# Performance work log

Measured on AMD Instinct MI355X. Metric: run time of the kernel, lower is better.

Reference implementation:

```python
import jax, jax.numpy as jnp
import numpy as np
import math

EPS = 1e-6
KP = -1.0  # Poincare ball curvature (c=1 -> kappa=-1)
KS = 1.0   # stereographic sphere projection (c=1 -> kappa=+1)

def _n(x):
    return jnp.sqrt(jnp.sum(x * x, -1, keepdims=True) + 1e-15)

def tan_k(u, k):
    if k < 0:
        return jnp.tanh(u)
    return jnp.tan(jnp.clip(u, -1.47079, 1.47079))

def artan_k(u, k):
    if k < 0:
        return jnp.arctanh(jnp.clip(u, -1 + 1e-5, 1 - 1e-5))
    return jnp.arctan(u)

def proj(x, k):
    if k < 0:
        n = _n(x)
        m = 1.0 - 1e-4
        return jnp.where(n > m, x * (m / n), x)
    return x

def expmap0(u, k):
    n = _n(u)
    return proj(tan_k(n, k) * u / n, k)

def logmap0(y, k):
    n = _n(y)
    return artan_k(n, k) * y / n

def _safe_den(d):
    return jnp.where(d >= 0, jnp.maximum(d, EPS), jnp.minimum(d, -EPS))

def mobius_add(x, y, k):
    x2 = jnp.sum(x * x, -1, keepdims=True)
    y2 = jnp.sum(y * y, -1, keepdims=True)
    xy = jnp.sum(x * y, -1, keepdims=True)
    num = (1 - 2 * k * xy - k * y2) * x + (1 + k * x2) * y
    den = 1 - 2 * k * xy + k * k * x2 * y2
    return proj(num / _safe_den(den), k)

def mobius_pw_mul(w, x, k):
    wx = w * x
    nx = _n(x)
    nwx = _n(wx)
    return proj(tan_k(nwx / nx * artan_k(nx, k), k) * wx / nwx, k)

def mobius_smul(r, x, k):
    n = _n(x)
    return proj(tan_k(r * artan_k(n, k), k) * x / n, k)

def wmid(xs, k, axis, w=None):
    lam = 2.0 / (1.0 + k * jnp.sum(xs * xs, -1, keepdims=True))
    if w is None:
        w = jnp.ones_like(lam)
    num = jnp.sum(w * lam * xs, axis=axis)
    den = jnp.abs(jnp.sum(w * (lam - 1.0), axis=axis))
    return mobius_smul(0.5, num / jnp.maximum(den, EPS), k)

def slin(x, W, b, k=None):
    if k is None:
        return x @ W.T + b
    return expmap0(logmap0(x, k) @ W.T + b, k)

def dist(x, y, k):
    return 2.0 * artan_k(_n(mobius_add(-x, y, k))[..., 0], k)

def hyp_attn(kk, q, v, k):
    # kk, v: [N,K,h]; q: [N,h]
    sc = -dist(q[:, None, :], kk, k)              # [N,K]
    a = jax.nn.softmax(sc, axis=1)[..., None]
    return wmid(v, k, axis=1, w=a)

def euc_attn(kk, q, v):
    sc = jnp.einsum('nkh,nh->nk', kk, q) / math.sqrt(kk.shape[-1])
    a = jax.nn.softmax(sc, axis=1)
    return jnp.einsum('nk,nkh->nh', a, v)


def _forward(x, h1, c1, h2, c2, h3, c3, del_t, iou1, iou2, iou3,
             Wq_w, Wq_b, Wc_w, Wc_b, Uf_w, Uf_b, Up_w, Up_b,
             Uiou_w, Uiou_b, d, nbr):
    sg, th = jax.nn.sigmoid, jnp.tanh
    # mailbox gather (message_func + DGL mailbox), [N,K,h]
    mh1, mh2, mh3 = h1[nbr], h2[nbr], h3[nbr]
    mc1, mc2, mc3 = c1[nbr], c2[nbr], c3[nbr]
    g_t = (d / (del_t[nbr] + 1.0))[..., None]      # [N,K,1]

    x_1p = slin(expmap0(x, KP), Wq_w, Wq_b, KP)
    x_1s = slin(expmap0(x, KS), Wq_w, Wq_b, KS)
    x_1e = slin(x, Wq_w, Wq_b)

    s1 = logmap0(sg(slin(mh1, Up_w, Up_b, KP)), KP)
    s2 = logmap0(sg(slin(mh2, Up_w, Up_b, KS)), KS)
    s3 = sg(slin(mh3, Up_w, Up_b))

    ht1p = mobius_pw_mul(s1, mh1, KP)
    ht2p = mobius_pw_mul(s2, expmap0(logmap0(mh2, KS), KP), KP)
    ht3p = mobius_pw_mul(s3, expmap0(mh3, KP), KP)
    h_1p = 3.0 * wmid(jnp.stack([ht1p, ht2p, ht3p]), KP, axis=0)

    ht1s = mobius_pw_mul(s1, expmap0(logmap0(mh1, KP), KS), KP)
    ht2s = mobius_pw_mul(s2, mh2, KS)
    ht3s = mobius_pw_mul(s3, expmap0(mh3, KS), KS)
    h_1s = 3.0 * wmid(jnp.stack([ht1s, ht2s, ht3s]), KP, axis=0)

    ht1e = logmap0(mobius_pw_mul(s1, mh1, KP), KP)
    ht2e = logmap0(mobius_pw_mul(s2, mh2, KS), KS)
    h_1e = ht1e + ht2e + s3 * mh3

    h_tildp = hyp_attn(h_1p, x_1p, h_1p, KP)
    h_tilds = hyp_attn(h_1s, x_1s, h_1s, KS)
    h_tilde = euc_attn(h_1e, x_1e, h_1e)

    # Poincare cell path
    csk_p = expmap0(th(logmap0(slin(mc1, Wc_w, Wc_b, KP), KP)), KP)
    ckt_p = mobius_add(mobius_add(-csk_p, mc1, KP), mobius_pw_mul(csk_p, g_t, KP), KP)
    f_p = sg(logmap0(slin(mh1, Uf_w, Uf_b, KP), KP))
    c_1 = wmid(mobius_pw_mul(f_p, ckt_p, KP), KP, axis=1)

    # Sphere cell path
    csk_s = expmap0(th(logmap0(slin(mc2, Wc_w, Wc_b, KS), KS)), KS)
    ckt_s = mobius_add(mobius_add(-csk_s, mc2, KS), mobius_pw_mul(csk_s, g_t, KS), KS)
    f_s = sg(logmap0(slin(mh2, Uf_w, Uf_b, KS), KS))
    c_2 = wmid(mobius_pw_mul(f_s, ckt_s, KS), KS, axis=1)

    # Euclidean cell path
    csk_e = th(slin(mc3, Wc_w, Wc_b))
    ckt_e = mc3 - csk_e + csk_e * g_t
    f_e = sg(slin(mh3, Uf_w, Uf_b))
    c_3 = jnp.sum(f_e * ckt_e, 1)

    niou1 = mobius_add(iou1, slin(h_tildp, Uiou_w, Uiou_b, KP), KP)
    niou2 = mobius_add(iou2, slin(h_tilds, Uiou_w, Uiou_b, KS), KS)
    niou3 = iou3 + slin(h_tilde, Uiou_w, Uiou_b)

    # apply_node_func
    i_p, o_p, u_p = jnp.split(niou1, 3, axis=1)
    i_p, o_p, u_p = sg(logmap0(i_p, KP)), sg(logmap0(o_p, KP)), th(logmap0(u_p, KP))
    i_s, o_s, u_s = jnp.split(niou2, 3, axis=1)
    i_s, o_s, u_s = sg(logmap0(i_s, KS)), sg(logmap0(o_s, KS)), th(logmap0(u_s, KS))
    i_e, o_e, u_e = jnp.split(niou3, 3, axis=1)
    i_e, o_e, u_e = sg(i_e), sg(o_e), th(u_e)

    nc1 = mobius_add(mobius_pw_mul(i_p, u_p, KP), c_1, KP)
    nc2 = mobius_add(mobius_pw_mul(i_s, u_s, KS), c_2, KS)
    nc3 = i_e * u_e + c_3
    nh1 = mobius_pw_mul(o_p, th(logmap0(nc1, KP)), KP)
    nh2 = mobius_pw_mul(o_s, th(logmap0(nc2, KS)), KS)
    nh3 = o_e * th(nc3)
    return jnp.stack([nh1, nc1, nh2, nc2, nh3, nc3])  # [6,N,h]


def setup_inputs() -> dict:
    N, K, H, X = 8192, 8, 128, 128
    key = jax.random.key(0)
    ks = jax.random.split(key, 24)
    def rn(i, shape, sc=0.05):
        return sc * jax.random.normal(ks[i], shape, jnp.float32)
    return dict(
        x=rn(0, (N, X)), h1=rn(1, (N, H)), c1=rn(2, (N, H)),
        h2=rn(3, (N, H)), c2=rn(4, (N, H)), h3=rn(5, (N, H)), c3=rn(6, (N, H)),
        del_t=jax.random.uniform(ks[7], (N,), jnp.float32),
        iou1=rn(8, (N, 3 * H)), iou2=rn(9, (N, 3 * H)), iou3=rn(10, (N, 3 * H)),
        Wq_w=rn(11, (H, X)), Wq_b=rn(12, (H,), 0.01),
        Wc_w=rn(13, (H, H)), Wc_b=rn(14, (H,), 0.01),
        Uf_w=rn(15, (H, H)), Uf_b=rn(16, (H,), 0.01),
        Up_w=rn(17, (H, H)), Up_b=rn(18, (H,), 0.01),
        Uiou_w=rn(19, (3 * H, H)), Uiou_b=rn(20, (3 * H,), 0.01),
        d=jnp.asarray(60.0, jnp.float32),
        nbr=jax.random.randint(ks[21], (N, K), 0, N),
    )


def reference(x, h1, c1, h2, c2, h3, c3, del_t, iou1, iou2, iou3,
              Wq_w, Wq_b, Wc_w, Wc_b, Uf_w, Uf_b, Up_w, Up_b,
              Uiou_w, Uiou_b, d, nbr):
    return _forward(x, h1, c1, h2, c2, h3, c3, del_t, iou1, iou2, iou3,
                    Wq_w, Wq_b, Wc_w, Wc_b, Uf_w, Uf_b, Up_w, Up_b,
                    Uiou_w, Uiou_b, d, nbr)
```

## Files before the change

### kernel.cpp

```cpp
#include <hip/hip_runtime.h>
#include <math.h>

#define HD 128
#define NNODE 8192
#define KNBR 8
#define NHS ((size_t)NNODE*(size_t)HD)

#define EPSF 1e-6f
#define PMX 0.9999f
#define ATHC (1.0f-1e-5f)
#define TANC 1.47079f

typedef unsigned short u16;
typedef unsigned int u32;
typedef _Float16 f16;
typedef __attribute__((ext_vector_type(8))) short short8;
typedef __attribute__((ext_vector_type(4))) float f32x4;
typedef __attribute__((ext_vector_type(2))) float f32x2;
typedef __attribute__((ext_vector_type(2))) _Float16 f16x2;
typedef __attribute__((ext_vector_type(4))) _Float16 f16x4;

static __device__ __forceinline__ float frcp(float x){ return __builtin_amdgcn_rcpf(x); }
static __device__ __forceinline__ float fdiv(float a,float b){ return a*__builtin_amdgcn_rcpf(b); }
static __device__ __forceinline__ float fsqrt(float x){ return __builtin_amdgcn_sqrtf(x); }
static __device__ __forceinline__ float fexp(float x){ return __builtin_amdgcn_exp2f(x*1.4426950408889634f); }
static __device__ __forceinline__ float flog(float x){ return __builtin_amdgcn_logf(x)*0.6931471805599453f; }
static __device__ __forceinline__ float ftanh(float x){
  float ax = fabsf(x);
  float e = fexp(-2.0f*ax);
  float t = (1.0f-e)*frcp(1.0f+e);
  return copysignf(t,x);
}
static __device__ __forceinline__ float fatanh(float x){
  x = fminf(fmaxf(x,-ATHC),ATHC);
  return 0.5f*flog((1.0f+x)*frcp(1.0f-x));
}
static __device__ __forceinline__ float fatan(float x){
  float ax = fabsf(x);
  bool inv = ax > 1.0f;
  float t = inv ? frcp(ax) : ax;
  float t2 = t*t;
  float p = -0.0117212f;
  p = p*t2 + 0.05265332f;
  p = p*t2 - 0.11643287f;
  p = p*t2 + 0.19354346f;
  p = p*t2 - 0.33262347f;
  p = p*t2 + 0.99997726f;
  float r = t*p;
  r = inv ? 1.5707963267948966f - r : r;
  return copysignf(r,x);
}
static __device__ __forceinline__ float ftan(float x){
  x = fminf(fmaxf(x,-TANC),TANC);
  float r = x*0.15915494309189535f;
  float s = __builtin_amdgcn_sinf(r);
  float c = __builtin_amdgcn_cosf(r);
  return s*frcp(c);
}
static __device__ __forceinline__ float sigm(float x){ return frcp(1.0f+fexp(-x)); }
static __device__ __forceinline__ float safeden(float d){
  return d>=0.0f ? fmaxf(d,EPSF) : fminf(d,-EPSF);
}

static __device__ __forceinline__ float wred(float v){
#pragma unroll
  for(int m=32;m;m>>=1) v += __shfl_xor(v,m,64);
  return v;
}
static __device__ __forceinline__ float hred16(float v){
#pragma unroll
  for(int m=8;m;m>>=1) v += __shfl_xor(v,m,64);
  return v;
}

static __device__ __forceinline__ u16 f2bf(float f){
  u32 u = __float_as_uint(f);
  u32 r = u + 0x7fffu + ((u>>16)&1u);
  return (u16)(r>>16);
}
static __device__ __forceinline__ float bf2f(u16 h){
  return __uint_as_float(((u32)h)<<16);
}
static __device__ __forceinline__ void split2x2(float v0, float v1, u16* hp, u16* lp){
  u16 h0 = f2bf(v0), h1 = f2bf(v1);
  float r0 = v0 - bf2f(h0), r1 = v1 - bf2f(h1);
  *(u32*)hp = (u32)h0 | ((u32)h1<<16);
  *(u32*)lp = (u32)f2bf(r0) | ((u32)f2bf(r1)<<16);
}

static __device__ __forceinline__ f32x2 ldh2(const u16* p){
  f16x2 v = *(const f16x2*)p;
  return (f32x2){(float)v[0], (float)v[1]};
}
static __device__ __forceinline__ void sth2(u16* p, float a, float b){
  *(f16x2*)p = (f16x2){(f16)a, (f16)b};
}

#define SCOFF (27*NHS)
#define WOFF  (27*NHS + 49152)
#define NW    114688

__global__ __launch_bounds__(256) void k_pre(
    const float* __restrict__ x, const float* __restrict__ h1,
    const float* __restrict__ h2, const float* __restrict__ c1,
    const float* __restrict__ c2, const float* __restrict__ h3,
    const float* __restrict__ c3,
    const float* __restrict__ Wq, const float* __restrict__ Wc,
    const float* __restrict__ Uf, const float* __restrict__ Up,
    const float* __restrict__ Uiou, float* __restrict__ ws)
{
  if(blockIdx.x >= 2048){
    u16* WH = (u16*)(ws + WOFF);
    u16* WL = WH + NW;
    int idx0 = ((blockIdx.x-2048)*256 + threadIdx.x)*4;
#pragma unroll
    for(int q=0;q<4;q+=2){
      int idx = idx0 + q;
      float v0, v1;
      if(idx < 16384)      { v0=Wq[idx]; v1=Wq[idx+1]; }
      else if(idx < 32768) { v0=Wc[idx-16384]; v1=Wc[idx-16383]; }
      else if(idx < 49152) { v0=Uf[idx-32768]; v1=Uf[idx-32767]; }
      else if(idx < 65536) { v0=Up[idx-49152]; v1=Up[idx-49151]; }
      else                 { v0=Uiou[idx-65536]; v1=Uiou[idx-65535]; }
      split2x2(v0, v1, &WH[idx], &WL[idx]);
    }
    return;
  }
  int row = blockIdx.x*4 + (threadIdx.x>>6);
  int l = threadIdx.x & 63;
  size_t i0 = (size_t)row*HD + 2*l;
#define LD2(p) (*(const f32x2*)&p[i0])
  f32x2 xv = LD2(x);
  f32x2 h1v = LD2(h1), h2v = LD2(h2), h3v = LD2(h3);
  f32x2 c1v = LD2(c1), c2v = LD2(c2), c3v = LD2(c3);
#undef LD2
  float xa=xv[0], xb=xv[1];
  float h1a=h1v[0], h1b=h1v[1];
  float h2a=h2v[0], h2b=h2v[1];
  float c1a=c1v[0], c1b=c1v[1];
  float c2a=c2v[0], c2b=c2v[1];
  float h3a=h3v[0], h3b=h3v[1];
  float c3a=c3v[0], c3b=c3v[1];
  float xsq = wred(xa*xa+xb*xb);
  float h1sq = wred(h1a*h1a+h1b*h1b);
  float h2sq = wred(h2a*h2a+h2b*h2b);
  float c1sq = wred(c1a*c1a+c1b*c1b);
  float c2sq = wred(c2a*c2a+c2b*c2b);
  size_t p0 = i0;
#define WRSPLIT(R, va, vb) { \
    u16* hp = (u16*)(ws + (size_t)(R)*NHS); u16* lp2 = hp + NHS; \
    split2x2(va, vb, &hp[p0], &lp2[p0]); }
  float nx = fsqrt(xsq+1e-15f);
  {
    float t = ftanh(nx);
    float f = fminf(t,PMX)*frcp(nx);
    float ny = fsqrt(f*f*xsq + 1e-15f);
    float g = fatanh(ny)*frcp(ny) * f;
    WRSPLIT(0, g*xa, g*xb)
  }
  {
    float t = ftan(nx);
    float f = t*frcp(nx);
    float ny = fsqrt(f*f*xsq + 1e-15f);
    float g = fatan(ny)*frcp(ny) * f;
    WRSPLIT(1, g*xa, g*xb)
  }
  WRSPLIT(2, xa, xb)
  { float n=fsqrt(h1sq+1e-15f); float g=fatanh(n)*frcp(n); WRSPLIT(3, g*h1a, g*h1b) }
  { float n=fsqrt(h2sq+1e-15f); float g=fatan(n)*frcp(n);  WRSPLIT(4, g*h2a, g*h2b) }
  WRSPLIT(5, h3a, h3b)
  { float n=fsqrt(c1sq+1e-15f); float g=fatanh(n)*frcp(n); WRSPLIT(6, g*c1a, g*c1b) }
  { float n=fsqrt(c2sq+1e-15f); float g=fatan(n)*frcp(n);  WRSPLIT(7, g*c2a, g*c2b) }
  WRSPLIT(8, c3a, c3b)
#undef WRSPLIT
}

enum { P_ID=0, P_EXP_P, P_EXP_S, P_SIG, P_TANH, P_SIG_LOG_P, P_SIG_LOG_S,
       P_LOGSIG_P, P_LOGSIG_S, P_TANH_EXP_P, P_TANH_EXP_S };

struct JobM { const u16* Ah; const u16* Al; const u16* Wh; const u16* Wl;
              const float* b; u16* out; int pitch; int post; };
struct JobTabM { JobM j[12]; };

__global__ __launch_bounds__(512) void k_gemmM(JobTabM tab){
  JobM jb = tab.j[blockIdx.y];
  __shared__ u16 Wlds[2*8*4*64*8];
  const int tid = threadIdx.x;
  const int lane = tid & 63;
  const int wave = tid >> 6;
  const int nn = lane & 15, quad = lane >> 4;
  const int row0 = blockIdx.x*128 + wave*16;
  const u16* Ah = jb.Ah + (size_t)(row0+nn)*128 + quad*8;
  const u16* Al = jb.Al + (size_t)(row0+nn)*128 + quad*8;
  short8 ah[4], al[4];
#pragma unroll
  for(int kk=0;kk<4;kk++){
    ah[kk] = *(const short8*)(Ah + kk*32);
    al[kk] = *(const short8*)(Al + kk*32);
  }
  for(int c = tid; c < 4096; c += 512){
    int lane_ = c & 63;
    int kk    = (c>>6)&3;
    int t     = (c>>8)&7;
    int plane = (c>>11)&1;
    const u16* src = (plane ? jb.Wl : jb.Wh)
                   + (size_t)(t*16 + (lane_&15))*128 + (lane_>>4)*8 + kk*32;
    *(uint4*)&Wlds[(size_t)c*8] = *(const uint4*)src;
  }
  float bias[8];
#pragma unroll
  for(int t=0;t<8;t++) bias[t] = jb.b[t*16+nn];
  __syncthreads();
  {
    f32x4 acc[8];
#pragma unroll
    for(int t=0;t<8;t++) acc[t] = (f32x4){0.f,0.f,0.f,0.f};
#pragma unroll
    for(int kk=0;kk<4;kk++){
#pragma unroll
      for(int t=0;t<8;t++){
        short8 wh = *(const short8*)&Wlds[(((0*8 + t)*4 + kk)*64 + lane)*8];
        short8 wl = *(const short8*)&Wlds[(((1*8 + t)*4 + kk)*64 + lane)*8];
        acc[t] = __builtin_amdgcn_mfma_f32_16x16x32_bf16(ah[kk], wh, acc[t], 0,0,0);
        acc[t] = __builtin_amdgcn_mfma_f32_16x16x32_bf16(al[kk], wh, acc[t], 0,0,0);
        acc[t] = __builtin_amdgcn_mfma_f32_16x16x32_bf16(ah[kk], wl, acc[t], 0,0,0);
      }
    }
#pragma unroll
    for(int r=0;r<4;r++){
      float v[8];
#pragma unroll
      for(int t=0;t<8;t++) v[t] = acc[t][r] + bias[t];
      float s2 = 0.f;
#pragma unroll
      for(int t=0;t<8;t++) s2 += v[t]*v[t];
      float nraw = hred16(s2);
      switch(jb.post){
        case P_ID: break;
        case P_EXP_P: {
          float n=fsqrt(nraw+1e-15f); float tt=ftanh(n); float f=fminf(tt,PMX)*frcp(n);
          for(int t=0;t<8;t++) v[t]*=f;
        } break;
        case P_EXP_S: {
          float n=fsqrt(nraw+1e-15f); float f=ftan(n)*frcp(n);
          for(int t=0;t<8;t++) v[t]*=f;
        } break;
        case P_SIG:
          for(int t=0;t<8;t++) v[t]=sigm(v[t]);
          break;
        case P_TANH:
          for(int t=0;t<8;t++) v[t]=ftanh(v[t]);
          break;
        case P_SIG_LOG_P: {
          float n=fsqrt(nraw+1e-15f); float tt=ftanh(n); float f=fminf(tt,PMX)*frcp(n);
          float z[8]; float zs=0.f;
          for(int t=0;t<8;t++){ z[t]=sigm(f*v[t]); zs+=z[t]*z[t]; }
          float zr=hred16(zs);
          float zn=fsqrt(zr+1e-15f);
          float g=fatanh(zn)*frcp(zn);
          for(int t=0;t<8;t++) v[t]=g*z[t];
        } break;
        case P_SIG_LOG_S: {
          float n=fsqrt(nraw+1e-15f); float f=ftan(n)*frcp(n);
          float z[8]; float zs=0.f;
          for(int t=0;t<8;t++){ z[t]=sigm(f*v[t]); zs+=z[t]*z[t]; }
          float zr=hred16(zs);
          float zn=fsqrt(zr+1e-15f);
          float g=fatan(zn)*frcp(zn);
          for(int t=0;t<8;t++) v[t]=g*z[t];
        } break;
        case P_LOGSIG_P: {
          float n=fsqrt(nraw+1e-15f); float tt=ftanh(n); float f=fminf(tt,PMX)*frcp(n);
          float ny=fsqrt(f*f*nraw+1e-15f);
          float g=fatanh(ny)*frcp(ny)*f;
          for(int t=0;t<8;t++) v[t]=sigm(g*v[t]);
        } break;
        case P_LOGSIG_S: {
          float n=fsqrt(nraw+1e-15f); float f=ftan(n)*frcp(n);
          float ny=fsqrt(f*f*nraw+1e-15f);
          float g=fatan(ny)*frcp(ny)*f;
          for(int t=0;t<8;t++) v[t]=sigm(g*v[t]);
        } break;
        case P_TANH_EXP_P: {
          float n=fsqrt(nraw+1e-15f); float tt=ftanh(n); float f=fminf(tt,PMX)*frcp(n);
          float ny=fsqrt(f*f*nraw+1e-15f);
          float g=fatanh(ny)*frcp(ny)*f;
          float T[8]; float Ts=0.f;
          for(int t=0;t<8;t++){ T[t]=ftanh(g*v[t]); Ts+=T[t]*T[t]; }
          float Tr=hred16(Ts);
          float Tn=fsqrt(Tr+1e-15f);
          float t2=ftanh(Tn); float f2=fminf(t2,PMX)*frcp(Tn);
          for(int t=0;t<8;t++) v[t]=f2*T[t];
        } break;
        case P_TANH_EXP_S: {
          float n=fsqrt(nraw+1e-15f); float f=ftan(n)*frcp(n);
          float ny=fsqrt(f*f*nraw+1e-15f);
          float g=fatan(ny)*frcp(ny)*f;
          float T[8]; float Ts=0.f;
          for(int t=0;t<8;t++){ T[t]=ftanh(g*v[t]); Ts+=T[t]*T[t]; }
          float Tr=hred16(Ts);
          float Tn=fsqrt(Tr+1e-15f);
          float f2=ftan(Tn)*frcp(Tn);
          for(int t=0;t<8;t++) v[t]=f2*T[t];
        } break;
      }
      u16* orow = jb.out + (size_t)(row0 + quad*4 + r)*jb.pitch + nn;
#pragma unroll
      for(int t=0;t<8;t++) *(f16*)&orow[t*16] = (f16)v[t];
// ... 99 lines not shown
  float v1xa,v1xb,d1v;
  {
    float q1sq = wred(q1a*q1a+q1b*q1b);
    float c1rs = wred(c1a*c1a+c1b*c1b);
    float dq1 = wred(q1a*c1a+q1b*c1b);
    float xy = -dq1;
    float aa = 1.0f+2.0f*xy+c1rs, bb = 1.0f-q1sq;
    float dd = frcp(safeden(1.0f+2.0f*xy+q1sq*c1rs));
    float m1a = (aa*(-q1a)+bb*c1a)*dd, m1b = (aa*(-q1b)+bb*c1b)*dd;
    float m1sq = (aa*aa*q1sq + 2.0f*aa*bb*xy + bb*bb*c1rs)*dd*dd;
    float mdq = (-aa*q1sq + bb*dq1)*dd;
    { float nm = fsqrt(m1sq+1e-15f);
      if(nm>PMX){ float sc=PMX*frcp(nm); m1a*=sc; m1b*=sc; m1sq*=sc*sc; mdq*=sc; } }
    float nwg = fsqrt(g*g*q1sq+1e-15f);
    float tg = ftanh(nwg*frcp(ng) * fatanh(ng));
    float fX = fminf(tg,PMX)*frcp(nwg) * g;
    float X2sq = fX*fX*q1sq;
    float xy2 = fX*mdq;
    float a2 = 1.0f+2.0f*xy2+X2sq, b2 = 1.0f-m1sq;
    float d2d = frcp(safeden(1.0f+2.0f*xy2+m1sq*X2sq));
    float ka = (a2*m1a + b2*fX*q1a)*d2d, kb = (a2*m1b + b2*fX*q1b)*d2d;
    float ksq = (a2*a2*m1sq + 2.0f*a2*b2*xy2 + b2*b2*X2sq)*d2d*d2d;
    { float nk0 = fsqrt(ksq+1e-15f);
      if(nk0>PMX){ float sc=PMX*frcp(nk0); ka*=sc; kb*=sc; ksq*=sc*sc; } }
    float nk = fsqrt(ksq+1e-15f);
    float wfa = f1a*ka, wfb = f1b*kb;
    float wfsq = wred(wfa*wfa+wfb*wfb); float nwf = fsqrt(wfsq+1e-15f);
    float tu = ftanh(nwf*frcp(nk) * fatanh(nk));
    float fu = fminf(tu,PMX)*frcp(nwf);
    float u1sq = fu*fu*wfsq;
    float lam = 2.0f*frcp(1.0f-u1sq);
    v1xa=lam*fu*wfa; v1xb=lam*fu*wfb;
    d1v=lam-1.0f;
  }
  float v2xa,v2xb,d2v;
  {
    float q2sq = wred(q2a*q2a+q2b*q2b);
    float c2rs = wred(c2a*c2a+c2b*c2b);
    float dq2 = wred(q2a*c2a+q2b*c2b);
    float xy = -dq2;
    float aa = 1.0f-2.0f*xy-c2rs, bb = 1.0f+q2sq;
    float dd = frcp(safeden(1.0f-2.0f*xy+q2sq*c2rs));
    float ma = (aa*(-q2a)+bb*c2a)*dd, mb = (aa*(-q2b)+bb*c2b)*dd;
    float msq = (aa*aa*q2sq + 2.0f*aa*bb*xy + bb*bb*c2rs)*dd*dd;
    float mdq = (-aa*q2sq + bb*dq2)*dd;
    float nwg = fsqrt(g*g*q2sq+1e-15f);
    float tg = ftan(nwg*frcp(ng) * fatan(ng));
    float fX = tg*frcp(nwg) * g;
    float X2sq = fX*fX*q2sq;
    float xy2 = fX*mdq;
    float a2 = 1.0f-2.0f*xy2-X2sq, b2 = 1.0f+msq;
    float d2d = frcp(safeden(1.0f-2.0f*xy2+msq*X2sq));
    float ka = (a2*ma + b2*fX*q2a)*d2d, kb = (a2*mb + b2*fX*q2b)*d2d;
    float ksq = (a2*a2*msq + 2.0f*a2*b2*xy2 + b2*b2*X2sq)*d2d*d2d;
    float nk = fsqrt(ksq+1e-15f);
    float wfa = f2a*ka, wfb = f2b*kb;
    float wfsq = wred(wfa*wfa+wfb*wfb); float nwf = fsqrt(wfsq+1e-15f);
    float tu = ftan(nwf*frcp(nk) * fatan(nk));
    float fu = tu*frcp(nwf);
    float u2sq = fu*fu*wfsq;
    float lam = 2.0f*frcp(1.0f+u2sq);
    v2xa=lam*fu*wfa; v2xb=lam*fu*wfb;
    d2v=lam-1.0f;
  }
  float v3xa,v3xb;
  {
    float kea = c3a + q3a*(g-1.0f), keb = c3b + q3b*(g-1.0f);
    v3xa=f3a*kea; v3xb=f3b*keb;
  }
  PKV4[pix] = (f16x4){(f16)v1xa,(f16)v1xb,(f16)v2xa,(f16)v2xb};
  PKV2[pix] = (f16x2){(f16)v3xa,(f16)v3xb};
  if(l==0) SC4[j] = (f32x4){y2pv,y2sv,d1v,d2v};
}

__global__ __launch_bounds__(256) void k_attn(
  const int* __restrict__ nbr, float* __restrict__ ws)
{
  const f16x2* PKP = (const f16x2*)(ws+21*NHS);
  const f16x2* PKS = (const f16x2*)(ws+22*NHS);
  const f16x2* PKE = (const f16x2*)(ws+23*NHS);
  const f16x4* PKV4= (const f16x4*)(ws+24*NHS);
  const f16x2* PKV2= (const f16x2*)(ws+26*NHS);
  const float* SCf = ws+SCOFF;
  u16* LPh = (u16*)(ws+9*NHS);  u16* LPl = LPh + NHS;
  u16* LSh = (u16*)(ws+10*NHS); u16* LSl = LSh + NHS;
  u16* LEh = (u16*)(ws+11*NHS); u16* LEl = LEh + NHS;
  u16* C1o = (u16*)(ws+12*NHS); u16* C2o = (u16*)(ws+13*NHS); u16* C3o = (u16*)(ws+14*NHS);
  float* c1n2 = ws+SCOFF+32768; float* c2n2 = ws+SCOFF+40960;

  int n = blockIdx.x;
  int wv = threadIdx.x>>6;
  int l = threadIdx.x&63;
  size_t i0 = (size_t)n*HD + 2*l;
  int4 jA = ((const int4*)nbr)[n*2+0];
  int4 jB = ((const int4*)nbr)[n*2+1];
  int js[8] = {jA.x,jA.y,jA.z,jA.w,jB.x,jB.y,jB.z,jB.w};

  if(wv==0){
    const u16* XP = (const u16*)(ws+18*NHS);
    f32x2 xv = ldh2(&XP[i0]);
    float XPa=xv[0], XPb=xv[1];
    float x2p = wred(XPa*XPa+XPb*XPb);
    float Ha[8],Hb[8],y2k[8];
#pragma unroll
    for(int k=0;k<8;k++){
      int j = js[k];
      f16x2 h = PKP[(size_t)j*64+l];
      Ha[k]=(float)h[0]; Hb[k]=(float)h[1];
      y2k[k]=SCf[(size_t)j*4+0];
    }
    float sc[8];
#pragma unroll
    for(int k=0;k<8;k++){
      float dp = wred(XPa*Ha[k]+XPb*Hb[k]);
      float xy=-dp, y2=y2k[k];
      float aa=1.0f+2.0f*xy+y2, bb=1.0f-x2p;
      float dd=frcp(safeden(1.0f+2.0f*xy+x2p*y2));
      float nsq=(aa*aa*x2p+2.0f*aa*bb*xy+bb*bb*y2)*dd*dd;
      float nn=fminf(fsqrt(nsq+1e-15f),PMX);
      sc[k] = -2.0f*fatanh(nn);
    }
    float mx=sc[0];
#pragma unroll
    for(int k=1;k<8;k++) mx=fmaxf(mx,sc[k]);
    float a[8]; float s=0;
#pragma unroll
    for(int k=0;k<8;k++){ a[k]=fexp(sc[k]-mx); s+=a[k]; }
    float inv=frcp(s);
    float na=0,nb=0,de=0;
#pragma unroll
    for(int k=0;k<8;k++){
      float lam = 2.0f*frcp(1.0f-y2k[k]); float w=a[k]*inv;
      na+=w*lam*Ha[k]; nb+=w*lam*Hb[k]; de+=w*(lam-1.0f);
    }
    de = frcp(fmaxf(fabsf(de),EPSF));
    na*=de; nb*=de;
    float vsq=wred(na*na+nb*nb); float nv=fsqrt(vsq+1e-15f);
    float tt=ftanh(0.5f*fatanh(nv)); float f=fminf(tt,PMX)*frcp(nv);
    float ha=f*na, hb=f*nb;
    float hn=fsqrt(f*f*vsq+1e-15f);
    float gl=fatanh(hn)*frcp(hn);
    split2x2(gl*ha, gl*hb, &LPh[i0], &LPl[i0]);
  } else if(wv==1){
    const u16* XS = (const u16*)(ws+19*NHS);
    f32x2 xv = ldh2(&XS[i0]);
    float XSa=xv[0], XSb=xv[1];
    float x2s = wred(XSa*XSa+XSb*XSb);
    float Ha[8],Hb[8],y2k[8];
#pragma unroll
    for(int k=0;k<8;k++){
      int j = js[k];
      f16x2 h = PKS[(size_t)j*64+l];
      Ha[k]=(float)h[0]; Hb[k]=(float)h[1];
      y2k[k]=SCf[(size_t)j*4+1];
    }
    float sc[8];
#pragma unroll
    for(int k=0;k<8;k++){
      float dsv = wred(XSa*Ha[k]+XSb*Hb[k]);
      float xy=-dsv, y2=y2k[k];
      float aa=1.0f-2.0f*xy-y2, bb=1.0f+x2s;
      float dd=frcp(safeden(1.0f-2.0f*xy+x2s*y2));
      float nsq=(aa*aa*x2s+2.0f*aa*bb*xy+bb*bb*y2)*dd*dd;
      float nn=fsqrt(nsq+1e-15f);
      sc[k] = -2.0f*fatan(nn);
    }
    float mx=sc[0];
#pragma unroll
    for(int k=1;k<8;k++) mx=fmaxf(mx,sc[k]);
    float a[8]; float s=0;
#pragma unroll
    for(int k=0;k<8;k++){ a[k]=fexp(sc[k]-mx); s+=a[k]; }
    float inv=frcp(s);
    float na=0,nb=0,de=0;
#pragma unroll
    for(int k=0;k<8;k++){
      float lam = 2.0f*frcp(1.0f+y2k[k]); float w=a[k]*inv;
      na+=w*lam*Ha[k]; nb+=w*lam*Hb[k]; de+=w*(lam-1.0f);
    }
    de = frcp(fmaxf(fabsf(de),EPSF));
    na*=de; nb*=de;
    float vsq=wred(na*na+nb*nb); float nv=fsqrt(vsq+1e-15f);
    float tt=ftan(0.5f*fatan(nv)); float f=tt*frcp(nv);
    float ha=f*na, hb=f*nb;
    float hn=fsqrt(f*f*vsq+1e-15f);
    float gl=fatan(hn)*frcp(hn);
    split2x2(gl*ha, gl*hb, &LSh[i0], &LSl[i0]);
  } else if(wv==2){
    const u16* XE = (const u16*)(ws+20*NHS);
    const float rs = 0.08838834764831845f;
    f32x2 xv = ldh2(&XE[i0]);
    float XEa=xv[0], XEb=xv[1];
    float Ha[8],Hb[8];
#pragma unroll
    for(int k=0;k<8;k++){
      int j = js[k];
      f16x2 h = PKE[(size_t)j*64+l];
      Ha[k]=(float)h[0]; Hb[k]=(float)h[1];
    }
    float sc[8];
#pragma unroll
    for(int k=0;k<8;k++) sc[k] = wred(XEa*Ha[k]+XEb*Hb[k])*rs;
    float mx=sc[0];
#pragma unroll
    for(int k=1;k<8;k++) mx=fmaxf(mx,sc[k]);
    float a[8]; float s=0;
#pragma unroll
    for(int k=0;k<8;k++){ a[k]=fexp(sc[k]-mx); s+=a[k]; }
    float inv=frcp(s);
    float ha=0,hb=0;
#pragma unroll
    for(int k=0;k<8;k++){ float w=a[k]*inv; ha+=w*Ha[k]; hb+=w*Hb[k]; }
    split2x2(ha, hb, &LEh[i0], &LEl[i0]);
  } else {
    float v1a=0,v1b=0,v2a=0,v2b=0,v3a=0,v3b=0,ds1=0,ds2=0;
#pragma unroll
    for(int k=0;k<8;k++){
      int j = js[k];
      f16x4 v4 = PKV4[(size_t)j*64+l];
      f16x2 v2 = PKV2[(size_t)j*64+l];
      v1a+=(float)v4[0]; v1b+=(float)v4[1]; v2a+=(float)v4[2]; v2b+=(float)v4[3];
      v3a+=(float)v2[0]; v3b+=(float)v2[1];
      ds1+=SCf[(size_t)j*4+2]; ds2+=SCf[(size_t)j*4+3];
    }
    {
      float de=frcp(fmaxf(fabsf(ds1),EPSF));
      float na=v1a*de, nb=v1b*de;
      float vsq=wred(na*na+nb*nb); float nv=fsqrt(vsq+1e-15f);
      float tt=ftanh(0.5f*fatanh(nv)); float f=fminf(tt,PMX)*frcp(nv);
      sth2(&C1o[i0], f*na, f*nb);
      if(l==0) c1n2[n]=f*f*vsq;
    }
    {
      float de=frcp(fmaxf(fabsf(ds2),EPSF));
      float na=v2a*de, nb=v2b*de;
      float vsq=wred(na*na+nb*nb); float nv=fsqrt(vsq+1e-15f);
      float tt=ftan(0.5f*fatan(nv)); float f=tt*frcp(nv);
      sth2(&C2o[i0], f*na, f*nb);
      if(l==0) c2n2[n]=f*f*vsq;
    }
    sth2(&C3o[i0], v3a, v3b);
  }
}

__global__ __launch_bounds__(256) void k_final(
  const float* __restrict__ iou1, const float* __restrict__ iou2,
  const float* __restrict__ iou3, float* __restrict__ ws,
  float* __restrict__ out)
{
  const u16* YP = (const u16*)ws;
  const u16* YS = (const u16*)(ws+3*NHS);
  const u16* YE = (const u16*)(ws+6*NHS);
  const u16* C1v = (const u16*)(ws+12*NHS);
  const u16* C2v = (const u16*)(ws+13*NHS);
  const u16* C3v = (const u16*)(ws+14*NHS);
  const float* c1n2 = ws+SCOFF+32768; const float* c2n2 = ws+SCOFF+40960;
  int n = blockIdx.x*4 + (threadIdx.x>>6);
  int l = threadIdx.x&63;
  size_t b384 = (size_t)n*384 + 2*l;
  size_t b128 = (size_t)n*HD + 2*l;
  {
    float Y[6], I[6];
#pragma unroll
    for(int p=0;p<3;p++){
      f32x2 yv = ldh2(&YP[b384 + 128*p]);
      f32x2 iv = *(const f32x2*)&iou1[b384 + 128*p];
      Y[2*p]=yv[0]; Y[2*p+1]=yv[1]; I[2*p]=iv[0]; I[2*p+1]=iv[1];
    }
    float sy=0,si=0,sx=0;
#pragma unroll
    for(int r=0;r<6;r++){ sy+=Y[r]*Y[r]; si+=I[r]*I[r]; sx+=I[r]*Y[r]; }
    sy=wred(sy); si=wred(si); sx=wred(sx);
    float nY=fsqrt(sy+1e-15f);
    float te=ftanh(nY); float fE=fminf(te,PMX)*frcp(nY);
    float y2=fE*fE*sy, x2=si, xy=fE*sx;
    float aa=1.0f+2.0f*xy+y2, bb=1.0f-x2;
    float dd=frcp(safeden(1.0f+2.0f*xy+x2*y2));
    float nio[6];
#pragma unroll
    for(int r=0;r<6;r++) nio[r]=(aa*I[r]+bb*fE*Y[r])*dd;
    float nsq=(aa*aa*x2+2.0f*aa*bb*xy+bb*bb*y2)*dd*dd;
    { float nn=fsqrt(nsq+1e-15f);
      if(nn>PMX){ float sc=PMX*frcp(nn); for(int r=0;r<6;r++) nio[r]*=sc; } }
    float ci=wred(nio[0]*nio[0]+nio[1]*nio[1]); float ni=fsqrt(ci+1e-15f); float gi=fatanh(ni)*frcp(ni);
    float ip0=sigm(gi*nio[0]), ip1=sigm(gi*nio[1]);
    float co=wred(nio[2]*nio[2]+nio[3]*nio[3]); float no=fsqrt(co+1e-15f); float go=fatanh(no)*frcp(no);
    float op0=sigm(go*nio[2]), op1=sigm(go*nio[3]);
    float cu=wred(nio[4]*nio[4]+nio[5]*nio[5]); float nu=fsqrt(cu+1e-15f); float gu=fatanh(nu)*frcp(nu);
    float up0=ftanh(gu*nio[4]), up1=ftanh(gu*nio[5]);
    float usq=wred(up0*up0+up1*up1); float nx=fsqrt(usq+1e-15f);
    float wv0=ip0*up0, wv1=ip1*up1;
    float wsq=wred(wv0*wv0+wv1*wv1); float nwx=fsqrt(wsq+1e-15f);
    float tP=ftanh(nwx*frcp(nx)*fatanh(nx)); float fP=fminf(tP,PMX)*frcp(nwx);
    float P0=fP*wv0, P1=fP*wv1; float p2=fP*fP*wsq;
    f32x2 cv = ldh2(&C1v[b128]);
    float ca=cv[0], cb=cv[1];
// ... 39 lines not shown
    float ip0=sigm(gi*nio[0]), ip1=sigm(gi*nio[1]);
    float co=wred(nio[2]*nio[2]+nio[3]*nio[3]); float no=fsqrt(co+1e-15f); float go=fatan(no)*frcp(no);
    float op0=sigm(go*nio[2]), op1=sigm(go*nio[3]);
    float cu=wred(nio[4]*nio[4]+nio[5]*nio[5]); float nu=fsqrt(cu+1e-15f); float gu=fatan(nu)*frcp(nu);
    float up0=ftanh(gu*nio[4]), up1=ftanh(gu*nio[5]);
    float usq=wred(up0*up0+up1*up1); float nx=fsqrt(usq+1e-15f);
    float wv0=ip0*up0, wv1=ip1*up1;
    float wsq=wred(wv0*wv0+wv1*wv1); float nwx=fsqrt(wsq+1e-15f);
    float tP=ftan(nwx*frcp(nx)*fatan(nx)); float fP=tP*frcp(nwx);
    float P0=fP*wv0, P1=fP*wv1; float p2=fP*fP*wsq;
    f32x2 cv = ldh2(&C2v[b128]);
    float ca=cv[0], cb=cv[1];
    float y2c=c2n2[n];
    float xyc=wred(P0*ca+P1*cb);
    float a3=1.0f-2.0f*xyc-y2c, b3=1.0f+p2;
    float d3=frcp(safeden(1.0f-2.0f*xyc+p2*y2c));
    float nc0=(a3*P0+b3*ca)*d3, nc1_=(a3*P1+b3*cb)*d3;
    float ncsq=(a3*a3*p2+2.0f*a3*b3*xyc+b3*b3*y2c)*d3*d3;
    float nl=fsqrt(ncsq+1e-15f);
    float gL=fatan(nl)*frcp(nl);
    float T0=ftanh(gL*nc0), T1=ftanh(gL*nc1_);
    float tsq=wred(T0*T0+T1*T1); float nT=fsqrt(tsq+1e-15f);
    float wo0=op0*T0, wo1=op1*T1;
    float osq=wred(wo0*wo0+wo1*wo1); float nwo=fsqrt(osq+1e-15f);
    float tH=ftan(nwo*frcp(nT)*fatan(nT)); float fH=tH*frcp(nwo);
    *(f32x2*)&out[2*NHS + b128] = (f32x2){fH*wo0, fH*wo1};
    *(f32x2*)&out[3*NHS + b128] = (f32x2){nc0, nc1_};
  }
  {
    float Y[6], I[6];
#pragma unroll
    for(int p=0;p<3;p++){
      f32x2 yv = ldh2(&YE[b384 + 128*p]);
      f32x2 iv = *(const f32x2*)&iou3[b384 + 128*p];
      Y[2*p]=yv[0]; Y[2*p+1]=yv[1]; I[2*p]=iv[0]; I[2*p+1]=iv[1];
    }
    float n0=I[0]+Y[0], n1=I[1]+Y[1];
    float n2=I[2]+Y[2], n3=I[3]+Y[3];
    float n4=I[4]+Y[4], n5=I[5]+Y[5];
    float ie0=sigm(n0), ie1=sigm(n1);
    float oe0=sigm(n2), oe1=sigm(n3);
    float ue0=ftanh(n4), ue1=ftanh(n5);
    f32x2 cv = ldh2(&C3v[b128]);
    float ca=cv[0], cb=cv[1];
    float nc0=ie0*ue0+ca, nc1_=ie1*ue1+cb;
    *(f32x2*)&out[4*NHS + b128] = (f32x2){oe0*ftanh(nc0), oe1*ftanh(nc1_)};
    *(f32x2*)&out[5*NHS + b128] = (f32x2){nc0, nc1_};
  }
}

extern "C" void kernel_launch(void* const* d_in, const int* in_sizes, int n_in,
                              void* d_out, int out_size, void* d_ws, size_t ws_size,
                              hipStream_t stream)
{
  const float* x     = (const float*)d_in[0];
  const float* h1    = (const float*)d_in[1];
  const float* c1    = (const float*)d_in[2];
  const float* h2    = (const float*)d_in[3];
  const float* c2    = (const float*)d_in[4];
  const float* h3    = (const float*)d_in[5];
  const float* c3    = (const float*)d_in[6];
  const float* del_t = (const float*)d_in[7];
  const float* iou1  = (const float*)d_in[8];
  const float* iou2  = (const float*)d_in[9];
  const float* iou3  = (const float*)d_in[10];
  const float* Wq_w  = (const float*)d_in[11];
  const float* Wq_b  = (const float*)d_in[12];
  const float* Wc_w  = (const float*)d_in[13];
  const float* Wc_b  = (const float*)d_in[14];
  const float* Uf_w  = (const float*)d_in[15];
  const float* Uf_b  = (const float*)d_in[16];
  const float* Up_w  = (const float*)d_in[17];
  const float* Up_b  = (const float*)d_in[18];
  const float* Uiou_w= (const float*)d_in[19];
  const float* Uiou_b= (const float*)d_in[20];
  const float* dsc   = (const float*)d_in[21];
  const int*   nbr   = (const int*)d_in[22];
  float* out = (float*)d_out;
  float* ws  = (float*)d_ws;

  k_pre<<<2160,256,0,stream>>>(x,h1,h2,c1,c2,h3,c3,Wq_w,Wc_w,Uf_w,Up_w,Uiou_w,ws);

  u16* WH = (u16*)(ws + WOFF);
  u16* WL = WH + NW;
  const u16* Wqh = WH;           const u16* Wql = WL;
  const u16* Wch = WH + 16384;   const u16* Wcl = WL + 16384;
  const u16* Ufh = WH + 32768;   const u16* Ufl = WL + 32768;
  const u16* Uph = WH + 49152;   const u16* Upl = WL + 49152;
  const u16* UIh = WH + 65536;   const u16* UIl = WL + 65536;
#define APLANE(R) ((const u16*)(ws + (size_t)(R)*NHS)), ((const u16*)(ws + (size_t)(R)*NHS) + NHS)

  JobTabM A{};
  A.j[0]  = { APLANE(0), Wqh, Wql, Wq_b, (u16*)(ws+18*NHS), 128, P_EXP_P };
  A.j[1]  = { APLANE(1), Wqh, Wql, Wq_b, (u16*)(ws+19*NHS), 128, P_EXP_S };
  A.j[2]  = { APLANE(2), Wqh, Wql, Wq_b, (u16*)(ws+20*NHS), 128, P_ID };
  A.j[3]  = { APLANE(3), Uph, Upl, Up_b, (u16*)(ws+9*NHS),  128, P_SIG_LOG_P };
  A.j[4]  = { APLANE(4), Uph, Upl, Up_b, (u16*)(ws+10*NHS), 128, P_SIG_LOG_S };
  A.j[5]  = { APLANE(5), Uph, Upl, Up_b, (u16*)(ws+11*NHS), 128, P_SIG };
  A.j[6]  = { APLANE(3), Ufh, Ufl, Uf_b, (u16*)(ws+12*NHS), 128, P_LOGSIG_P };
  A.j[7]  = { APLANE(4), Ufh, Ufl, Uf_b, (u16*)(ws+13*NHS), 128, P_LOGSIG_S };
  A.j[8]  = { APLANE(5), Ufh, Ufl, Uf_b, (u16*)(ws+14*NHS), 128, P_SIG };
  A.j[9]  = { APLANE(6), Wch, Wcl, Wc_b, (u16*)(ws+15*NHS), 128, P_TANH_EXP_P };
  A.j[10] = { APLANE(7), Wch, Wcl, Wc_b, (u16*)(ws+16*NHS), 128, P_TANH_EXP_S };
  A.j[11] = { APLANE(8), Wch, Wcl, Wc_b, (u16*)(ws+17*NHS), 128, P_TANH };
  k_gemmM<<<dim3(NNODE/128,12),512,0,stream>>>(A);

  k_phaseB<<<2048,256,0,stream>>>(h1,h2,h3,c1,c2,c3,del_t,dsc,ws);
  k_attn<<<8192,256,0,stream>>>(nbr,ws);

  JobTabM B{};
  for(int ct=0; ct<3; ct++){
    B.j[0*3+ct] = { APLANE(9),  UIh + ct*16384, UIl + ct*16384, Uiou_b + ct*128, (u16*)(ws+0*NHS) + ct*128, 384, P_ID };
    B.j[1*3+ct] = { APLANE(10), UIh + ct*16384, UIl + ct*16384, Uiou_b + ct*128, (u16*)(ws+3*NHS) + ct*128, 384, P_ID };
    B.j[2*3+ct] = { APLANE(11), UIh + ct*16384, UIl + ct*16384, Uiou_b + ct*128, (u16*)(ws+6*NHS) + ct*128, 384, P_ID };
  }
  k_gemmM<<<dim3(NNODE/128,9),512,0,stream>>>(B);

  k_final<<<2048,256,0,stream>>>(iou1,iou2,iou3,ws,out);
}
```

Before: 250.5 us.

## Replace split-bf16 three-pass GEMM emulation with single fp16 MFMA

```diff
diff --git a/kernel.cpp b/kernel.cpp
--- a/kernel.cpp
+++ b/kernel.cpp
@@ -14,11 +14,11 @@
 typedef unsigned short u16;
 typedef unsigned int u32;
 typedef _Float16 f16;
-typedef __attribute__((ext_vector_type(8))) short short8;
 typedef __attribute__((ext_vector_type(4))) float f32x4;
 typedef __attribute__((ext_vector_type(2))) float f32x2;
 typedef __attribute__((ext_vector_type(2))) _Float16 f16x2;
 typedef __attribute__((ext_vector_type(4))) _Float16 f16x4;
+typedef __attribute__((ext_vector_type(8))) _Float16 f16x8;
 
 static __device__ __forceinline__ float frcp(float x){ return __builtin_amdgcn_rcpf(x); }
 static __device__ __forceinline__ float fdiv(float a,float b){ return a*__builtin_amdgcn_rcpf(b); }
@@ -73,21 +73,6 @@
   return v;
 }
 
-static __device__ __forceinline__ u16 f2bf(float f){
-  u32 u = __float_as_uint(f);
-  u32 r = u + 0x7fffu + ((u>>16)&1u);
-  return (u16)(r>>16);
-}
-static __device__ __forceinline__ float bf2f(u16 h){
-  return __uint_as_float(((u32)h)<<16);
-}
-static __device__ __forceinline__ void split2x2(float v0, float v1, u16* hp, u16* lp){
-  u16 h0 = f2bf(v0), h1 = f2bf(v1);
-  float r0 = v0 - bf2f(h0), r1 = v1 - bf2f(h1);
-  *(u32*)hp = (u32)h0 | ((u32)h1<<16);
-  *(u32*)lp = (u32)f2bf(r0) | ((u32)f2bf(r1)<<16);
-}
-
 static __device__ __forceinline__ f32x2 ldh2(const u16* p){
   f16x2 v = *(const f16x2*)p;
   return (f32x2){(float)v[0], (float)v[1]};
@@ -111,7 +96,6 @@
 {
   if(blockIdx.x >= 2048){
     u16* WH = (u16*)(ws + WOFF);
-    u16* WL = WH + NW;
     int idx0 = ((blockIdx.x-2048)*256 + threadIdx.x)*4;
 #pragma unroll
     for(int q=0;q<4;q+=2){
@@ -122,7 +106,7 @@
       else if(idx < 49152) { v0=Uf[idx-32768]; v1=Uf[idx-32767]; }
       else if(idx < 65536) { v0=Up[idx-49152]; v1=Up[idx-49151]; }
       else                 { v0=Uiou[idx-65536]; v1=Uiou[idx-65535]; }
-      split2x2(v0, v1, &WH[idx], &WL[idx]);
+      sth2(&WH[idx], v0, v1);
     }
     return;
   }
@@ -147,64 +131,55 @@
   float c1sq = wred(c1a*c1a+c1b*c1b);
   float c2sq = wred(c2a*c2a+c2b*c2b);
   size_t p0 = i0;
-#define WRSPLIT(R, va, vb) { \
-    u16* hp = (u16*)(ws + (size_t)(R)*NHS); u16* lp2 = hp + NHS; \
-    split2x2(va, vb, &hp[p0], &lp2[p0]); }
+#define WRF16(R, va, vb) sth2(&((u16*)(ws + (size_t)(R)*NHS))[p0], va, vb);
   float nx = fsqrt(xsq+1e-15f);
   {
     float t = ftanh(nx);
     float f = fminf(t,PMX)*frcp(nx);
     float ny = fsqrt(f*f*xsq + 1e-15f);
     float g = fatanh(ny)*frcp(ny) * f;
-    WRSPLIT(0, g*xa, g*xb)
+    WRF16(0, g*xa, g*xb)
   }
   {
     float t = ftan(nx);
     float f = t*frcp(nx);
     float ny = fsqrt(f*f*xsq + 1e-15f);
     float g = fatan(ny)*frcp(ny) * f;
-    WRSPLIT(1, g*xa, g*xb)
-  }
-  WRSPLIT(2, xa, xb)
-  { float n=fsqrt(h1sq+1e-15f); float g=fatanh(n)*frcp(n); WRSPLIT(3, g*h1a, g*h1b) }
-  { float n=fsqrt(h2sq+1e-15f); float g=fatan(n)*frcp(n);  WRSPLIT(4, g*h2a, g*h2b) }
-  WRSPLIT(5, h3a, h3b)
-  { float n=fsqrt(c1sq+1e-15f); float g=fatanh(n)*frcp(n); WRSPLIT(6, g*c1a, g*c1b) }
-  { float n=fsqrt(c2sq+1e-15f); float g=fatan(n)*frcp(n);  WRSPLIT(7, g*c2a, g*c2b) }
-  WRSPLIT(8, c3a, c3b)
-#undef WRSPLIT
+    WRF16(1, g*xa, g*xb)
+  }
+  WRF16(2, xa, xb)
+  { float n=fsqrt(h1sq+1e-15f); float g=fatanh(n)*frcp(n); WRF16(3, g*h1a, g*h1b) }
+  { float n=fsqrt(h2sq+1e-15f); float g=fatan(n)*frcp(n);  WRF16(4, g*h2a, g*h2b) }
+  WRF16(5, h3a, h3b)
+  { float n=fsqrt(c1sq+1e-15f); float g=fatanh(n)*frcp(n); WRF16(6, g*c1a, g*c1b) }
+  { float n=fsqrt(c2sq+1e-15f); float g=fatan(n)*frcp(n);  WRF16(7, g*c2a, g*c2b) }
+  WRF16(8, c3a, c3b)
+#undef WRF16
 }
 
 enum { P_ID=0, P_EXP_P, P_EXP_S, P_SIG, P_TANH, P_SIG_LOG_P, P_SIG_LOG_S,
        P_LOGSIG_P, P_LOGSIG_S, P_TANH_EXP_P, P_TANH_EXP_S };
 
-struct JobM { const u16* Ah; const u16* Al; const u16* Wh; const u16* Wl;
-              const float* b; u16* out; int pitch; int post; };
+struct JobM { const u16* A; const u16* W; const float* b; u16* out; int pitch; int post; };
 struct JobTabM { JobM j[12]; };
 
 __global__ __launch_bounds__(512) void k_gemmM(JobTabM tab){
   JobM jb = tab.j[blockIdx.y];
-  __shared__ u16 Wlds[2*8*4*64*8];
+  __shared__ u16 Wlds[8*4*64*8];
   const int tid = threadIdx.x;
   const int lane = tid & 63;
   const int wave = tid >> 6;
   const int nn = lane & 15, quad = lane >> 4;
   const int row0 = blockIdx.x*128 + wave*16;
-  const u16* Ah = jb.Ah + (size_t)(row0+nn)*128 + quad*8;
-  const u16* Al = jb.Al + (size_t)(row0+nn)*128 + quad*8;
-  short8 ah[4], al[4];
-#pragma unroll
-  for(int kk=0;kk<4;kk++){
-    ah[kk] = *(const short8*)(Ah + kk*32);
-    al[kk] = *(const short8*)(Al + kk*32);
-  }
-  for(int c = tid; c < 4096; c += 512){
+  const u16* A = jb.A + (size_t)(row0+nn)*128 + quad*8;
+  f16x8 a[4];
+#pragma unroll
+  for(int kk=0;kk<4;kk++) a[kk] = *(const f16x8*)(A + kk*32);
+  for(int c = tid; c < 2048; c += 512){
     int lane_ = c & 63;
     int kk    = (c>>6)&3;
     int t     = (c>>8)&7;
-    int plane = (c>>11)&1;
-    const u16* src = (plane ? jb.Wl : jb.Wh)
-                   + (size_t)(t*16 + (lane_&15))*128 + (lane_>>4)*8 + kk*32;
+    const u16* src = jb.W + (size_t)(t*16 + (lane_&15))*128 + (lane_>>4)*8 + kk*32;
     *(uint4*)&Wlds[(size_t)c*8] = *(const uint4*)src;
   }
   float bias[8];
@@ -219,11 +194,8 @@
     for(int kk=0;kk<4;kk++){
 #pragma unroll
       for(int t=0;t<8;t++){
-        short8 wh = *(const short8*)&Wlds[(((0*8 + t)*4 + kk)*64 + lane)*8];
-        short8 wl = *(const short8*)&Wlds[(((1*8 + t)*4 + kk)*64 + lane)*8];
-        acc[t] = __builtin_amdgcn_mfma_f32_16x16x32_bf16(ah[kk], wh, acc[t], 0,0,0);
-        acc[t] = __builtin_amdgcn_mfma_f32_16x16x32_bf16(al[kk], wh, acc[t], 0,0,0);
-        acc[t] = __builtin_amdgcn_mfma_f32_16x16x32_bf16(ah[kk], wl, acc[t], 0,0,0);
+        f16x8 wh = *(const f16x8*)&Wlds[((t*4 + kk)*64 + lane)*8];
+        acc[t] = __builtin_amdgcn_mfma_f32_16x16x32_f16(a[kk], wh, acc[t], 0,0,0);
       }
     }
 #pragma unroll
@@ -489,9 +461,9 @@
   const f16x4* PKV4= (const f16x4*)(ws+24*NHS);
   const f16x2* PKV2= (const f16x2*)(ws+26*NHS);
   const float* SCf = ws+SCOFF;
-  u16* LPh = (u16*)(ws+9*NHS);  u16* LPl = LPh + NHS;
-  u16* LSh = (u16*)(ws+10*NHS); u16* LSl = LSh + NHS;
-  u16* LEh = (u16*)(ws+11*NHS); u16* LEl = LEh + NHS;
+  u16* LP = (u16*)(ws+9*NHS);
+  u16* LS = (u16*)(ws+10*NHS);
+  u16* LE = (u16*)(ws+11*NHS);
   u16* C1o = (u16*)(ws+12*NHS); u16* C2o = (u16*)(ws+13*NHS); u16* C3o = (u16*)(ws+14*NHS);
   float* c1n2 = ws+SCOFF+32768; float* c2n2 = ws+SCOFF+40960;
 
@@ -547,7 +519,7 @@
     float ha=f*na, hb=f*nb;
     float hn=fsqrt(f*f*vsq+1e-15f);
     float gl=fatanh(hn)*frcp(hn);
-    split2x2(gl*ha, gl*hb, &LPh[i0], &LPl[i0]);
+    sth2(&LP[i0], gl*ha, gl*hb);
   } else if(wv==1){
     const u16* XS = (const u16*)(ws+19*NHS);
     f32x2 xv = ldh2(&XS[i0]);
@@ -592,7 +564,7 @@
     float ha=f*na, hb=f*nb;
     float hn=fsqrt(f*f*vsq+1e-15f);
     float gl=fatan(hn)*frcp(hn);
-    split2x2(gl*ha, gl*hb, &LSh[i0], &LSl[i0]);
+    sth2(&LS[i0], gl*ha, gl*hb);
   } else if(wv==2){
     const u16* XE = (const u16*)(ws+20*NHS);
     const float rs = 0.08838834764831845f;
@@ -618,7 +590,7 @@
     float ha=0,hb=0;
 #pragma unroll
     for(int k=0;k<8;k++){ float w=a[k]*inv; ha+=w*Ha[k]; hb+=w*Hb[k]; }
-    split2x2(ha, hb, &LEh[i0], &LEl[i0]);
+    sth2(&LE[i0], ha, hb);
   } else {
     float v1a=0,v1b=0,v2a=0,v2b=0,v3a=0,v3b=0,ds1=0,ds2=0;
 #pragma unroll
@@ -824,27 +796,26 @@
   k_pre<<<2160,256,0,stream>>>(x,h1,h2,c1,c2,h3,c3,Wq_w,Wc_w,Uf_w,Up_w,Uiou_w,ws);
 
   u16* WH = (u16*)(ws + WOFF);
-  u16* WL = WH + NW;
-  const u16* Wqh = WH;           const u16* Wql = WL;
-  const u16* Wch = WH + 16384;   const u16* Wcl = WL + 16384;
-  const u16* Ufh = WH + 32768;   const u16* Ufl = WL + 32768;
-  const u16* Uph = WH + 49152;   const u16* Upl = WL + 49152;
-  const u16* UIh = WH + 65536;   const u16* UIl = WL + 65536;
-#define APLANE(R) ((const u16*)(ws + (size_t)(R)*NHS)), ((const u16*)(ws + (size_t)(R)*NHS) + NHS)
+  const u16* Wqh = WH;
+  const u16* Wch = WH + 16384;
+  const u16* Ufh = WH + 32768;
+  const u16* Uph = WH + 49152;
+  const u16* UIh = WH + 65536;
+#define APLANE(R) ((const u16*)(ws + (size_t)(R)*NHS))
 
   JobTabM A{};
-  A.j[0]  = { APLANE(0), Wqh, Wql, Wq_b, (u16*)(ws+18*NHS), 128, P_EXP_P };
-  A.j[1]  = { APLANE(1), Wqh, Wql, Wq_b, (u16*)(ws+19*NHS), 128, P_EXP_S };
-  A.j[2]  = { APLANE(2), Wqh, Wql, Wq_b, (u16*)(ws+20*NHS), 128, P_ID };
-  A.j[3]  = { APLANE(3), Uph, Upl, Up_b, (u16*)(ws+9*NHS),  128, P_SIG_LOG_P };
-  A.j[4]  = { APLANE(4), Uph, Upl, Up_b, (u16*)(ws+10*NHS), 128, P_SIG_LOG_S };
-  A.j[5]  = { APLANE(5), Uph, Upl, Up_b, (u16*)(ws+11*NHS), 128, P_SIG };
-  A.j[6]  = { APLANE(3), Ufh, Ufl, Uf_b, (u16*)(ws+12*NHS), 128, P_LOGSIG_P };
-  A.j[7]  = { APLANE(4), Ufh, Ufl, Uf_b, (u16*)(ws+13*NHS), 128, P_LOGSIG_S };
-  A.j[8]  = { APLANE(5), Ufh, Ufl, Uf_b, (u16*)(ws+14*NHS), 128, P_SIG };
-  A.j[9]  = { APLANE(6), Wch, Wcl, Wc_b, (u16*)(ws+15*NHS), 128, P_TANH_EXP_P };
-  A.j[10] = { APLANE(7), Wch, Wcl, Wc_b, (u16*)(ws+16*NHS), 128, P_TANH_EXP_S };
-  A.j[11] = { APLANE(8), Wch, Wcl, Wc_b, (u16*)(ws+17*NHS), 128, P_TANH };
+  A.j[0]  = { APLANE(0), Wqh, Wq_b, (u16*)(ws+18*NHS), 128, P_EXP_P };
+  A.j[1]  = { APLANE(1), Wqh, Wq_b, (u16*)(ws+19*NHS), 128, P_EXP_S };
+  A.j[2]  = { APLANE(2), Wqh, Wq_b, (u16*)(ws+20*NHS), 128, P_ID };
+  A.j[3]  = { APLANE(3), Uph, Up_b, (u16*)(ws+9*NHS),  128, P_SIG_LOG_P };
+  A.j[4]  = { APLANE(4), Uph, Up_b, (u16*)(ws+10*NHS), 128, P_SIG_LOG_S };
+  A.j[5]  = { APLANE(5), Uph, Up_b, (u16*)(ws+11*NHS), 128, P_SIG };
+  A.j[6]  = { APLANE(3), Ufh, Uf_b, (u16*)(ws+12*NHS), 128, P_LOGSIG_P };
+  A.j[7]  = { APLANE(4), Ufh, Uf_b, (u16*)(ws+13*NHS), 128, P_LOGSIG_S };
+  A.j[8]  = { APLANE(5), Ufh, Uf_b, (u16*)(ws+14*NHS), 128, P_SIG };
+  A.j[9]  = { APLANE(6), Wch, Wc_b, (u16*)(ws+15*NHS), 128, P_TANH_EXP_P };
+  A.j[10] = { APLANE(7), Wch, Wc_b, (u16*)(ws+16*NHS), 128, P_TANH_EXP_S };
+  A.j[11] = { APLANE(8), Wch, Wc_b, (u16*)(ws+17*NHS), 128, P_TANH };
   k_gemmM<<<dim3(NNODE/128,12),512,0,stream>>>(A);
 
   k_phaseB<<<2048,256,0,stream>>>(h1,h2,h3,c1,c2,c3,del_t,dsc,ws);
@@ -852,9 +823,9 @@
 
   JobTabM B{};
   for(int ct=0; ct<3; ct++){
-    B.j[0*3+ct] = { APLANE(9),  UIh + ct*16384, UIl + ct*16384, Uiou_b + ct*128, (u16*)(ws+0*NHS) + ct*128, 384, P_ID };
-    B.j[1*3+ct] = { APLANE(10), UIh + ct*16384, UIl + ct*16384, Uiou_b + ct*128, (u16*)(ws+3*NHS) + ct*128, 384, P_ID };
-    B.j[2*3+ct] = { APLANE(11), UIh + ct*16384, UIl + ct*16384, Uiou_b + ct*128, (u16*)(ws+6*NHS) + ct*128, 384, P_ID };
+    B.j[0*3+ct] = { APLANE(9),  UIh + ct*16384, Uiou_b + ct*128, (u16*)(ws+0*NHS) + ct*128, 384, P_ID };
+    B.j[1*3+ct] = { APLANE(10), UIh + ct*16384, Uiou_b + ct*128, (u16*)(ws+3*NHS) + ct*128, 384, P_ID };
+    B.j[2*3+ct] = { APLANE(11), UIh + ct*16384, Uiou_b + ct*128, (u16*)(ws+6*NHS) + ct*128, 384, P_ID };
   }
   k_gemmM<<<dim3(NNODE/128,9),512,0,stream>>>(B);
 
```

Result: faster. 226.4 us (median of 2 runs) (-9.6%).
